# Optimization experiments

Hardware: AMD Instinct MI355X
Metric: run time of the kernel (lower is better)

Reference implementation:

```python
import jax, jax.numpy as jnp
import numpy as np

DIM = 4096
LOG_DIM = int(np.log2(DIM))  # 12
BATCH = 8192


def setup_inputs() -> dict:
    key = jax.random.key(0)
    k1, k2, k3 = jax.random.split(key, 3)
    x = jax.random.normal(k1, (BATCH, DIM), dtype=jnp.float32)
    # packed per-layer rotation params: layer l has DIM >> (l+1) blocks;
    # total = DIM - 1 = 4095. Original init: a=cos(theta), b=sin(theta), theta~0.01*N(0,1)
    theta = jax.random.normal(k2, (DIM - 1,), dtype=jnp.float32) * 0.01
    a_flat = jnp.cos(theta)
    b_flat = jnp.sin(theta)
    del k3
    return {"x": x, "a_flat": a_flat, "b_flat": b_flat}


def reference(x, a_flat, b_flat):
    B, D = x.shape
    off = 0
    for layer in range(LOG_DIM):
        bs = 1 << layer                  # block_size = 2**layer
        nb = D // (2 * bs)               # num_blocks
        a = a_flat[off:off + nb][None, :, None]  # [1, nb, 1]
        b = b_flat[off:off + nb][None, :, None]
        off += nb
        xv = x.reshape(B, nb, 2, bs)
        x0 = xv[:, :, 0, :]
        x1 = xv[:, :, 1, :]
        top = a * x0 + b * x1
        bot = -b * x0 + a * x1
        x = jnp.stack([top, bot], axis=2).reshape(B, D)
    return x
```

## Files before the change

kernel.cpp:

```cpp
#include <hip/hip_runtime.h>

#define DIM   4096
#define BATCH 8192

#if defined(__has_builtin)
#  if __has_builtin(__builtin_amdgcn_permlane32_swap)
#    define HAVE_PL32 1
#  endif
#  if __has_builtin(__builtin_amdgcn_permlane16_swap)
#    define HAVE_PL16 1
#  endif
#endif
#ifndef HAVE_PL32
#  define HAVE_PL32 0
#endif
#ifndef HAVE_PL16
#  define HAVE_PL16 0
#endif

typedef float f32x4_v __attribute__((ext_vector_type(4)));

__device__ __forceinline__ void store_nt4(float4* p, const float4& v) {
    f32x4_v t; t.x = v.x; t.y = v.y; t.z = v.z; t.w = v.w;
    __builtin_nontemporal_store(t, reinterpret_cast<f32x4_v*>(p));
}

__device__ __forceinline__ void rot2(float& lo, float& hi, float a, float b) {
    float l = lo, h = hi;
    lo = fmaf(a, l,  b * h);
    hi = fmaf(a, h, -b * l);
}

template<int M>
__device__ __forceinline__ float pxor(float x, bool hi) {
    int xi = __float_as_int(x);
    if constexpr (M == 1)
        return __int_as_float(__builtin_amdgcn_update_dpp(0, xi, 0xB1, 0xF, 0xF, true));
    else if constexpr (M == 2)
        return __int_as_float(__builtin_amdgcn_update_dpp(0, xi, 0x4E, 0xF, 0xF, true));
    else if constexpr (M == 4)
        return __int_as_float(__builtin_amdgcn_ds_swizzle(xi, 0x101F));
    else if constexpr (M == 8)
        return __int_as_float(__builtin_amdgcn_update_dpp(0, xi, 0x128, 0xF, 0xF, true));
    else if constexpr (M == 16) {
#if HAVE_PL16
        unsigned xu = (unsigned)xi;
        auto r = __builtin_amdgcn_permlane16_swap(xu, xu, false, false);
        return __uint_as_float(hi ? r[0] : r[1]);
#else
        return __int_as_float(__builtin_amdgcn_ds_swizzle(xi, 0x401F));
#endif
    } else {
#if HAVE_PL32
        unsigned xu = (unsigned)xi;
        auto r = __builtin_amdgcn_permlane32_swap(xu, xu, false, false);
        return __uint_as_float(hi ? r[0] : r[1]);
#else
        return __shfl_xor(x, 32, 64);
#endif
    }
}

template<int M, int JSH, int LSH, bool UNIF>
__device__ __forceinline__ void shuf_layer(float4 (&v)[4], int lane, int base,
                                           const float* __restrict__ af,
                                           const float* __restrict__ bf) {
    const bool hi = (lane & M) != 0;
    #pragma unroll
    for (int j = 0; j < 4; ++j) {
        int c = base + (j << JSH) + (lane >> LSH);
        if constexpr (UNIF) c = __builtin_amdgcn_readfirstlane(c);
        const float a = af[c], b = bf[c];
        const float sb = hi ? -b : b;
        v[j].x = fmaf(a, v[j].x, sb * pxor<M>(v[j].x, hi));
        v[j].y = fmaf(a, v[j].y, sb * pxor<M>(v[j].y, hi));
        v[j].z = fmaf(a, v[j].z, sb * pxor<M>(v[j].z, hi));
        v[j].w = fmaf(a, v[j].w, sb * pxor<M>(v[j].w, hi));
    }
}

__global__ __launch_bounds__(256, 7)
void bfly_kernel(const float* __restrict__ x,
                 const float* __restrict__ af,
                 const float* __restrict__ bf,
                 float* __restrict__ out) {
    const int lane = threadIdx.x & 63;
    const int q    = threadIdx.x >> 6;
    const size_t row = blockIdx.x;

    const float4* __restrict__ xr = reinterpret_cast<const float4*>(x + row * DIM) + q * 256;
    float4* __restrict__ orow     = reinterpret_cast<float4*>(out + row * DIM) + q * 256;

    __shared__ float4 xch[4][4][64];

    float4 v[4];
    #pragma unroll
    for (int j = 0; j < 4; ++j) v[j] = xr[64 * j + lane];

    #pragma unroll
    for (int j = 0; j < 4; ++j) {
        const int c = 512 * q + 128 * j + 2 * lane;
        float2 aa = *reinterpret_cast<const float2*>(af + c);
        float2 bb = *reinterpret_cast<const float2*>(bf + c);
        rot2(v[j].x, v[j].y, aa.x, bb.x);
        rot2(v[j].z, v[j].w, aa.y, bb.y);
    }

    #pragma unroll
    for (int j = 0; j < 4; ++j) {
        const int c = 2048 + 256 * q + 64 * j + lane;
        const float a = af[c], b = bf[c];
        rot2(v[j].x, v[j].z, a, b);
        rot2(v[j].y, v[j].w, a, b);
    }

    shuf_layer< 1, 5, 1, false>(v, lane, 3072 + 128 * q, af, bf);
    shuf_layer< 2, 4, 2, false>(v, lane, 3584 +  64 * q, af, bf);
    shuf_layer< 4, 3, 3, false>(v, lane, 3840 +  32 * q, af, bf);
    shuf_layer< 8, 2, 4, false>(v, lane, 3968 +  16 * q, af, bf);
    shuf_layer<16, 1, 5, false>(v, lane, 4032 +   8 * q, af, bf);
    shuf_layer<32, 0, 6, true >(v, lane, 4064 +   4 * q, af, bf);

    #pragma unroll
    for (int k = 0; k < 2; ++k) {
        const int c = __builtin_amdgcn_readfirstlane(4080 + 2 * q + k);
        const float a = af[c], b = bf[c];
        rot2(v[2*k].x, v[2*k+1].x, a, b);
        rot2(v[2*k].y, v[2*k+1].y, a, b);
        rot2(v[2*k].z, v[2*k+1].z, a, b);
        rot2(v[2*k].w, v[2*k+1].w, a, b);
    }
    {
        const int c = __builtin_amdgcn_readfirstlane(4088 + q);
        const float a = af[c], b = bf[c];
        #pragma unroll
        for (int j = 0; j < 2; ++j) {
            rot2(v[j].x, v[j+2].x, a, b);
            rot2(v[j].y, v[j+2].y, a, b);
            rot2(v[j].z, v[j+2].z, a, b);
            rot2(v[j].w, v[j+2].w, a, b);
        }
    }

    {
        const float a0 = af[4092], b0 = bf[4092];
        const float a1 = af[4093], b1 = bf[4093];
        const float A  = af[4094], B  = bf[4094];
        const int h11 = q >> 1, h10 = q & 1;
        const float aO = h11 ? a1 : a0, bO = h11 ? b1 : b0;
        const float aX = h11 ? a0 : a1, bX = h11 ? b0 : b1;
        const float phX = h11 ? -B : B;
        const float w0 = A * aO;
        const float w1 = A * (h10 ? -bO : bO);
        const float w2 = phX * aX;
        const float w3 = phX * (h10 ? -bX : bX);
        const int q1 = q ^ 1, q2 = q ^ 2, q3 = q ^ 3;

        #pragma unroll
        for (int j = 0; j < 4; ++j) xch[q][j][lane] = v[j];
        __syncthreads();
        #pragma unroll
        for (int j = 0; j < 4; ++j) {
            float4 e1 = xch[q1][j][lane];
            float4 e2 = xch[q2][j][lane];
            float4 e3 = xch[q3][j][lane];
            float4 a;
            a.x = fmaf(w3, e3.x, fmaf(w2, e2.x, fmaf(w1, e1.x, w0 * v[j].x)));
            a.y = fmaf(w3, e3.y, fmaf(w2, e2.y, fmaf(w1, e1.y, w0 * v[j].y)));
            a.z = fmaf(w3, e3.z, fmaf(w2, e2.z, fmaf(w1, e1.z, w0 * v[j].z)));
            a.w = fmaf(w3, e3.w, fmaf(w2, e2.w, fmaf(w1, e1.w, w0 * v[j].w)));
            v[j] = a;
        }
    }

    #pragma unroll
    for (int j = 0; j < 4; ++j) store_nt4(&orow[64 * j + lane], v[j]);
}

extern "C" void kernel_launch(void* const* d_in, const int* in_sizes, int n_in,
                              void* d_out, int out_size, void* d_ws, size_t ws_size,
                              hipStream_t stream) {
    const float* x  = (const float*)d_in[0];
    const float* af = (const float*)d_in[1];
    const float* bf = (const float*)d_in[2];
    float* out      = (float*)d_out;
    (void)d_ws; (void)ws_size;

    hipLaunchKernelGGL(bfly_kernel, dim3(BATCH), dim3(256), 0, stream,
                       x, af, bf, out);
}
```

Baseline: 47.94 us.

## Process each row with two waves of 32 elements per lane instead of four

Each row is now handled by a 128-thread block of two wavefronts, each holding 8 float4 per lane. One more butterfly layer is therefore done in registers. The cross-wave LDS exchange shrinks from a 4-way combine of two fused layers to a simple 2-way rotation. This cuts LDS traffic and cross-wave arithmetic per element, but doubles register usage per thread and halves the threads per block, which may reduce occupancy and latency hiding for this memory-bound kernel.

```diff
diff --git a/kernel.cpp b/kernel.cpp
--- a/kernel.cpp
+++ b/kernel.cpp
@@ -29,6 +29,10 @@
     float l = lo, h = hi;
     lo = fmaf(a, l,  b * h);
     hi = fmaf(a, h, -b * l);
+}
+__device__ __forceinline__ void rot4(float4& lo, float4& hi, float a, float b) {
+    rot2(lo.x, hi.x, a, b); rot2(lo.y, hi.y, a, b);
+    rot2(lo.z, hi.z, a, b); rot2(lo.w, hi.w, a, b);
 }
 
 template<int M>
@@ -62,12 +66,12 @@
 }
 
 template<int M, int JSH, int LSH, bool UNIF>
-__device__ __forceinline__ void shuf_layer(float4 (&v)[4], int lane, int base,
+__device__ __forceinline__ void shuf_layer(float4 (&v)[8], int lane, int base,
                                            const float* __restrict__ af,
                                            const float* __restrict__ bf) {
     const bool hi = (lane & M) != 0;
     #pragma unroll
-    for (int j = 0; j < 4; ++j) {
+    for (int j = 0; j < 8; ++j) {
         int c = base + (j << JSH) + (lane >> LSH);
         if constexpr (UNIF) c = __builtin_amdgcn_readfirstlane(c);
         const float a = af[c], b = bf[c];
@@ -79,27 +83,27 @@
     }
 }
 
-__global__ __launch_bounds__(256, 7)
+__global__ __launch_bounds__(128)
 void bfly_kernel(const float* __restrict__ x,
                  const float* __restrict__ af,
                  const float* __restrict__ bf,
                  float* __restrict__ out) {
     const int lane = threadIdx.x & 63;
-    const int q    = threadIdx.x >> 6;
+    const int w    = threadIdx.x >> 6;
     const size_t row = blockIdx.x;
 
-    const float4* __restrict__ xr = reinterpret_cast<const float4*>(x + row * DIM) + q * 256;
-    float4* __restrict__ orow     = reinterpret_cast<float4*>(out + row * DIM) + q * 256;
+    const float4* __restrict__ xr = reinterpret_cast<const float4*>(x + row * DIM) + w * 512;
+    float4* __restrict__ orow     = reinterpret_cast<float4*>(out + row * DIM) + w * 512;
 
-    __shared__ float4 xch[4][4][64];
+    __shared__ float4 xch[2][8][64];
 
-    float4 v[4];
+    float4 v[8];
     #pragma unroll
-    for (int j = 0; j < 4; ++j) v[j] = xr[64 * j + lane];
+    for (int j = 0; j < 8; ++j) v[j] = xr[64 * j + lane];
 
     #pragma unroll
-    for (int j = 0; j < 4; ++j) {
-        const int c = 512 * q + 128 * j + 2 * lane;
+    for (int j = 0; j < 8; ++j) {
+        const int c = 1024 * w + 128 * j + 2 * lane;
         float2 aa = *reinterpret_cast<const float2*>(af + c);
         float2 bb = *reinterpret_cast<const float2*>(bf + c);
         rot2(v[j].x, v[j].y, aa.x, bb.x);
@@ -107,74 +111,57 @@
     }
 
     #pragma unroll
-    for (int j = 0; j < 4; ++j) {
-        const int c = 2048 + 256 * q + 64 * j + lane;
+    for (int j = 0; j < 8; ++j) {
+        const int c = 2048 + 512 * w + 64 * j + lane;
         const float a = af[c], b = bf[c];
         rot2(v[j].x, v[j].z, a, b);
         rot2(v[j].y, v[j].w, a, b);
     }
 
-    shuf_layer< 1, 5, 1, false>(v, lane, 3072 + 128 * q, af, bf);
-    shuf_layer< 2, 4, 2, false>(v, lane, 3584 +  64 * q, af, bf);
-    shuf_layer< 4, 3, 3, false>(v, lane, 3840 +  32 * q, af, bf);
-    shuf_layer< 8, 2, 4, false>(v, lane, 3968 +  16 * q, af, bf);
-    shuf_layer<16, 1, 5, false>(v, lane, 4032 +   8 * q, af, bf);
-    shuf_layer<32, 0, 6, true >(v, lane, 4064 +   4 * q, af, bf);
+    shuf_layer< 1, 5, 1, false>(v, lane, 3072 + 256 * w, af, bf);
+    shuf_layer< 2, 4, 2, false>(v, lane, 3584 + 128 * w, af, bf);
+    shuf_layer< 4, 3, 3, false>(v, lane, 3840 +  64 * w, af, bf);
+    shuf_layer< 8, 2, 4, false>(v, lane, 3968 +  32 * w, af, bf);
+    shuf_layer<16, 1, 5, false>(v, lane, 4032 +  16 * w, af, bf);
+    shuf_layer<32, 0, 6, true >(v, lane, 4064 +   8 * w, af, bf);
 
     #pragma unroll
-    for (int k = 0; k < 2; ++k) {
-        const int c = __builtin_amdgcn_readfirstlane(4080 + 2 * q + k);
+    for (int k = 0; k < 4; ++k) {
+        const int c = __builtin_amdgcn_readfirstlane(4080 + 4 * w + k);
+        rot4(v[2*k], v[2*k + 1], af[c], bf[c]);
+    }
+    #pragma unroll
+    for (int g = 0; g < 2; ++g) {
+        const int c = __builtin_amdgcn_readfirstlane(4088 + 2 * w + g);
         const float a = af[c], b = bf[c];
-        rot2(v[2*k].x, v[2*k+1].x, a, b);
-        rot2(v[2*k].y, v[2*k+1].y, a, b);
-        rot2(v[2*k].z, v[2*k+1].z, a, b);
-        rot2(v[2*k].w, v[2*k+1].w, a, b);
+        rot4(v[4*g],     v[4*g + 2], a, b);
+        rot4(v[4*g + 1], v[4*g + 3], a, b);
     }
     {
-        const int c = __builtin_amdgcn_readfirstlane(4088 + q);
+        const int c = __builtin_amdgcn_readfirstlane(4092 + w);
         const float a = af[c], b = bf[c];
         #pragma unroll
-        for (int j = 0; j < 2; ++j) {
-            rot2(v[j].x, v[j+2].x, a, b);
-            rot2(v[j].y, v[j+2].y, a, b);
-            rot2(v[j].z, v[j+2].z, a, b);
-            rot2(v[j].w, v[j+2].w, a, b);
-        }
+        for (int t = 0; t < 4; ++t) rot4(v[t], v[t + 4], a, b);
     }
 
     {
-        const float a0 = af[4092], b0 = bf[4092];
-        const float a1 = af[4093], b1 = bf[4093];
-        const float A  = af[4094], B  = bf[4094];
-        const int h11 = q >> 1, h10 = q & 1;
-        const float aO = h11 ? a1 : a0, bO = h11 ? b1 : b0;
-        const float aX = h11 ? a0 : a1, bX = h11 ? b0 : b1;
-        const float phX = h11 ? -B : B;
-        const float w0 = A * aO;
-        const float w1 = A * (h10 ? -bO : bO);
-        const float w2 = phX * aX;
-        const float w3 = phX * (h10 ? -bX : bX);
-        const int q1 = q ^ 1, q2 = q ^ 2, q3 = q ^ 3;
-
+        const float A = af[4094], B = bf[4094];
+        const float sb = w ? -B : B;
         #pragma unroll
-        for (int j = 0; j < 4; ++j) xch[q][j][lane] = v[j];
+        for (int j = 0; j < 8; ++j) xch[w][j][lane] = v[j];
         __syncthreads();
         #pragma unroll
-        for (int j = 0; j < 4; ++j) {
-            float4 e1 = xch[q1][j][lane];
-            float4 e2 = xch[q2][j][lane];
-            float4 e3 = xch[q3][j][lane];
-            float4 a;
-            a.x = fmaf(w3, e3.x, fmaf(w2, e2.x, fmaf(w1, e1.x, w0 * v[j].x)));
-            a.y = fmaf(w3, e3.y, fmaf(w2, e2.y, fmaf(w1, e1.y, w0 * v[j].y)));
-            a.z = fmaf(w3, e3.z, fmaf(w2, e2.z, fmaf(w1, e1.z, w0 * v[j].z)));
-            a.w = fmaf(w3, e3.w, fmaf(w2, e2.w, fmaf(w1, e1.w, w0 * v[j].w)));
-            v[j] = a;
+        for (int j = 0; j < 8; ++j) {
+            float4 p = xch[w ^ 1][j][lane];
+            v[j].x = fmaf(A, v[j].x, sb * p.x);
+            v[j].y = fmaf(A, v[j].y, sb * p.y);
+            v[j].z = fmaf(A, v[j].z, sb * p.z);
+            v[j].w = fmaf(A, v[j].w, sb * p.w);
         }
     }
 
     #pragma unroll
-    for (int j = 0; j < 4; ++j) store_nt4(&orow[64 * j + lane], v[j]);
+    for (int j = 0; j < 8; ++j) store_nt4(&orow[64 * j + lane], v[j]);
 }
 
 extern "C" void kernel_launch(void* const* d_in, const int* in_sizes, int n_in,
@@ -186,6 +173,6 @@
     float* out      = (float*)d_out;
     (void)d_ws; (void)ws_size;
 
-    hipLaunchKernelGGL(bfly_kernel, dim3(BATCH), dim3(256), 0, stream,
+    hipLaunchKernelGGL(bfly_kernel, dim3(BATCH), dim3(128), 0, stream,
                        x, af, bf, out);
 }
```

New measurement: 56.21 us. 1.17x slower.
